# Performance work log

Measured on AMD Instinct MI355X. Metric: run time of the kernel, lower is better.

The kernel has to match this reference:

```python
import jax, jax.numpy as jnp
import numpy as np

B, N, T, FM = 2, 768, 96, 8
HID = 64
TD = HID // 2   # temporal_dim = max(8, 32) = 32
MD = HID // 2   # mark_hidden_dim = 32


def _lin_init(key, fan_in, fan_out):
    k1, k2 = jax.random.split(key)
    bound = 1.0 / np.sqrt(fan_in)
    w = jax.random.uniform(k1, (fan_in, fan_out), minval=-bound, maxval=bound, dtype=jnp.float32)
    b = jax.random.uniform(k2, (fan_out,), minval=-bound, maxval=bound, dtype=jnp.float32)
    return w, b


def setup_inputs() -> dict:
    key = jax.random.key(0)
    ks = jax.random.split(key, 16)
    x_hist = jax.random.normal(ks[0], (B, N, T), dtype=jnp.float32)
    x_mark = jax.random.normal(ks[1], (B, N, T, FM), dtype=jnp.float32)
    a_static = jax.random.uniform(ks[2], (N, N), dtype=jnp.float32)
    te_w1, te_b1 = _lin_init(ks[3], 3, TD)
    te_w2, te_b2 = _lin_init(ks[4], TD, TD)
    me_w1, me_b1 = _lin_init(ks[5], FM, MD)
    me_w2, me_b2 = _lin_init(ks[6], MD, MD)
    nf_w, nf_b = _lin_init(ks[7], TD + MD, HID)
    ps_w1, ps_b1 = _lin_init(ks[8], 3 * HID, HID)
    ps_w2, ps_b2 = _lin_init(ks[9], HID, 1)
    raw_lambda = jnp.array([np.log(0.1 / 0.9)], dtype=jnp.float32)  # logit(lambda_init)
    return dict(x_hist=x_hist, x_mark=x_mark, a_static=a_static,
                te_w1=te_w1, te_b1=te_b1, te_w2=te_w2, te_b2=te_b2,
                me_w1=me_w1, me_b1=me_b1, me_w2=me_w2, me_b2=me_b2,
                nf_w=nf_w, nf_b=nf_b,
                ps_w1=ps_w1, ps_b1=ps_b1, ps_w2=ps_w2, ps_b2=ps_b2,
                raw_lambda=raw_lambda)


def reference(x_hist, x_mark, a_static,
              te_w1, te_b1, te_w2, te_b2,
              me_w1, me_b1, me_w2, me_b2,
              nf_w, nf_b, ps_w1, ps_b1, ps_w2, ps_b2, raw_lambda):
    n = x_hist.shape[1]
    # temporal stats: last / mean / max over T -> [B,N,3]
    stats = jnp.stack([x_hist[:, :, -1], x_hist.mean(axis=-1), x_hist.max(axis=-1)], axis=-1)
    h_t = jax.nn.relu(stats @ te_w1 + te_b1) @ te_w2 + te_b2          # [B,N,TD]
    mark_sum = x_mark.mean(axis=2)                                    # [B,N,FM]
    h_m = jax.nn.relu(mark_sum @ me_w1 + me_b1) @ me_w2 + me_b2       # [B,N,MD]
    h = jax.nn.relu(jnp.concatenate([h_t, h_m], axis=-1) @ nf_w + nf_b)  # [B,N,H]
    # pair scorer: Linear([h_i, h_j, |h_i-h_j|]) decomposed over the 3 blocks
    hdim = h.shape[-1]
    w_i, w_j, w_d = ps_w1[:hdim], ps_w1[hdim:2 * hdim], ps_w1[2 * hdim:]
    s_i = h @ w_i                                                     # [B,N,H]
    s_j = h @ w_j                                                     # [B,N,H]
    diff = jnp.abs(h[:, :, None, :] - h[:, None, :, :])               # [B,N,N,H]
    pre = s_i[:, :, None, :] + s_j[:, None, :, :] + diff @ w_d + ps_b1
    delta = jnp.tanh((jax.nn.relu(pre) @ ps_w2 + ps_b2)[..., 0])      # [B,N,N]
    eye = jnp.eye(n, dtype=delta.dtype)
    delta = delta * (1.0 - eye)
    delta = 0.5 * (delta + jnp.swapaxes(delta, 1, 2))                 # sym_graph
    lam = jax.nn.sigmoid(raw_lambda)                                  # [1]
    a_hybrid = a_static[None] + lam * delta
    a_hybrid = jax.nn.relu(a_hybrid)                                  # nonneg_mode='relu'
    d = jnp.clip(a_hybrid.sum(axis=-1, keepdims=True), 1e-6, None)    # row norm
    a_hybrid = a_hybrid / d
    return a_hybrid, lam
```

## Files before the change

kernel.cpp:

```cpp
#include <hip/hip_runtime.h>
#include <hip/hip_bf16.h>
#include <math.h>

#define B_ 2
#define N_ 768
#define T_ 96
#define FM_ 8
#define HID_ 64
#define TD_ 32
#define MD_ 32
#define TILE 16
#define TI32 32
#define NTILES (N_/TILE)
#define PERB 600
#define SSTR 68

typedef __attribute__((ext_vector_type(8))) short short8v;
typedef __attribute__((ext_vector_type(4))) float f32x4;
typedef __attribute__((ext_vector_type(4))) unsigned int uint4v;

__device__ __forceinline__ unsigned int pack_bf2(float d0, float d1){
  __hip_bfloat162 t = __float22bfloat162_rn(make_float2(d0, d1));
  unsigned int u;
  __builtin_memcpy(&u, &t, 4);
  return u;
}

__device__ __forceinline__ float ftanh(float x){
  float e = __expf(2.f * x);
  return 1.f - 2.f * __builtin_amdgcn_rcpf(e + 1.f);
}

__device__ __forceinline__ float wave_sum64(float v){
  #pragma unroll
  for (int m = 32; m; m >>= 1) v += __shfl_xor(v, m);
  return v;
}
__device__ __forceinline__ float wave_max64(float v){
  #pragma unroll
  for (int m = 32; m; m >>= 1) v = fmaxf(v, __shfl_xor(v, m));
  return v;
}

__global__ __launch_bounds__(64) void feat_kernel(
    const float* __restrict__ x_hist, const float* __restrict__ x_mark,
    const float* __restrict__ te_w1, const float* __restrict__ te_b1,
    const float* __restrict__ te_w2, const float* __restrict__ te_b2,
    const float* __restrict__ me_w1, const float* __restrict__ me_b1,
    const float* __restrict__ me_w2, const float* __restrict__ me_b2,
    const float* __restrict__ nf_w,  const float* __restrict__ nf_b,
    const float* __restrict__ ps_w1,
    float* __restrict__ h_out, float* __restrict__ si_out, float* __restrict__ sj_out,
    unsigned short* __restrict__ wdf)
{
  const int lane = threadIdx.x;

  if (blockIdx.x >= B_ * N_) {
    const int q  = blockIdx.x - B_ * N_;
    const int nt = q >> 1, s = q & 1;
    const int col = (lane & 15) + 16 * nt;
    const int k0  = s * 32 + ((lane >> 4) << 3);
    #pragma unroll
    for (int jj = 0; jj < 8; ++jj) {
      float v = ps_w1[(2 * HID_ + k0 + jj) * HID_ + col];
      __hip_bfloat16 bv = __float2bfloat16(v);
      unsigned short us;
      __builtin_memcpy(&us, &bv, 2);
      wdf[(q * 64 + lane) * 8 + jj] = us;
    }
    return;
  }

  const int row = blockIdx.x;

  __shared__ float st[3];
  __shared__ float ms[FM_];
  __shared__ float t1s[TD_];
  __shared__ float m1s[MD_];
  __shared__ float hc[HID_];
  __shared__ float hs[HID_];

  const float* xh = x_hist + (long)row * T_;
  float s  = xh[lane];
  float mx = s;
  if (lane < T_ - 64) { float v = xh[lane + 64]; s += v; mx = fmaxf(mx, v); }
  s  = wave_sum64(s);
  mx = wave_max64(mx);
  if (lane == 0) { st[0] = xh[T_ - 1]; st[1] = s * (1.0f / T_); st[2] = mx; }

  const float* xm = x_mark + (long)row * T_ * FM_;
  float msv = 0.f;
  #pragma unroll
  for (int k = 0; k < 12; ++k) msv += xm[lane + 64 * k];
  msv += __shfl_xor(msv, 8);
  msv += __shfl_xor(msv, 16);
  msv += __shfl_xor(msv, 32);
  if (lane < FM_) ms[lane] = msv * (1.0f / T_);
  __syncthreads();

  if (lane < TD_) {
    float a = te_b1[lane];
    #pragma unroll
    for (int k = 0; k < 3; ++k) a += st[k] * te_w1[k * TD_ + lane];
    t1s[lane] = fmaxf(a, 0.f);
    float am = me_b1[lane];
    #pragma unroll
    for (int k = 0; k < FM_; ++k) am += ms[k] * me_w1[k * MD_ + lane];
    m1s[lane] = fmaxf(am, 0.f);
  }
  __syncthreads();
  if (lane < TD_) {
    float a = te_b2[lane];
    #pragma unroll
    for (int k = 0; k < TD_; ++k) a += t1s[k] * te_w2[k * TD_ + lane];
    hc[lane] = a;
    float am = me_b2[lane];
    #pragma unroll
    for (int k = 0; k < MD_; ++k) am += m1s[k] * me_w2[k * MD_ + lane];
    hc[TD_ + lane] = am;
  }
  __syncthreads();
  {
    float a = nf_b[lane];
    #pragma unroll
    for (int k = 0; k < HID_; ++k) a += hc[k] * nf_w[k * HID_ + lane];
    float hv = fmaxf(a, 0.f);
    hs[lane] = hv;
    h_out[(long)row * HID_ + lane] = hv;
  }
  __syncthreads();
  {
    float a1 = 0.f, a2 = 0.f;
    #pragma unroll
    for (int k = 0; k < HID_; ++k) {
      float hv = hs[k];
      a1 += hv * ps_w1[k * HID_ + lane];
      a2 += hv * ps_w1[(HID_ + k) * HID_ + lane];
    }
    si_out[(long)row * HID_ + lane] = a1;
    sj_out[(long)row * HID_ + lane] = a2;
  }
}

__global__ __launch_bounds__(256, 3) void pair_kernel(
    const float* __restrict__ h, const float* __restrict__ si, const float* __restrict__ sj,
    const float* __restrict__ ps_b1, const float* __restrict__ ps_w2,
    const float* __restrict__ ps_b2, const unsigned short* __restrict__ wdf,
    float* __restrict__ delta)
{
  int bidx = blockIdx.x;
  int b = bidx / PERB;
  int t = bidx % PERB;
  int a = 0;
  while (t >= NTILES - 2 * a) { t -= NTILES - 2 * a; ++a; }
  int tJ = 2 * a + t;
  const int i0 = a * TI32, j0 = tJ * TILE;

  __shared__ float hI  [TI32][HID_];
  __shared__ float hJT [HID_][TILE + 1];
  __shared__ float SIIb[TI32][SSTR];
  __shared__ float SJI_[TI32][SSTR];
  __shared__ float SIJb[TILE][SSTR];
  __shared__ float SJJ_[TILE][SSTR];
  __shared__ float w2s [HID_];

  const int tid  = threadIdx.x;
  const int lane = tid & 63;
  const int w    = tid >> 6;

  {
    const int r  = tid >> 4;
    const int c4 = (tid & 15) * 4;
    const f32x4 b14 = *(const f32x4*)(ps_b1 + c4);
    #pragma unroll
    for (int p = 0; p < 2; ++p) {
      const int rr = r + p * 16;
      const long gi = ((long)b * N_ + i0 + rr) * HID_ + c4;
      *(f32x4*)&hI  [rr][c4] = *(const f32x4*)(h  + gi);
      *(f32x4*)&SIIb[rr][c4] = *(const f32x4*)(si + gi) + b14;
      *(f32x4*)&SJI_[rr][c4] = *(const f32x4*)(sj + gi);
    }
    const long gj = ((long)b * N_ + j0 + r) * HID_ + c4;
    f32x4 vhj = *(const f32x4*)(h + gj);
    #pragma unroll
    for (int q = 0; q < 4; ++q) hJT[c4 + q][r] = vhj[q];
    *(f32x4*)&SIJb[r][c4] = *(const f32x4*)(si + gj) + b14;
    *(f32x4*)&SJJ_[r][c4] = *(const f32x4*)(sj + gj);
    if (tid < 16) *(f32x4*)&w2s[tid * 4] = *(const f32x4*)(ps_w2 + tid * 4);
  }
  const float b2 = ps_b2[0];
  __syncthreads();

  const int g   = lane >> 4;
  const int c16 = lane & 15;

  short8v wfr[8];
  const short8v* wdp = (const short8v*)wdf;
  #pragma unroll
  for (int q = 0; q < 8; ++q) wfr[q] = wdp[q * 64 + lane];

  float hJv[2][8];
  #pragma unroll
  for (int s = 0; s < 2; ++s)
    #pragma unroll
    for (int jj = 0; jj < 8; ++jj)
      hJv[s][jj] = hJT[32 * s + 8 * g + jj][c16];

  f32x4 sJJ4h[4], sIJ4h[4], w24h[4];
  #pragma unroll
  for (int mt = 0; mt < 4; ++mt) {
    const int cb = 16 * mt + 4 * g;
    sJJ4h[mt] = *(const f32x4*)&SJJ_[c16][cb];
    sIJ4h[mt] = *(const f32x4*)&SIJb[c16][cb];
    w24h[mt]  = *(const f32x4*)&w2s[cb];
  }

  float* drow = delta + (long)b * N_ * N_;

  #pragma unroll
  for (int m = 0; m < 8; ++m) {
    const int iloc = w * 8 + m;
    const int i = i0 + iloc;

    short8v afr[2];
    #pragma unroll
    for (int s = 0; s < 2; ++s) {
      f32x4 ha = *(const f32x4*)&hI[iloc][32 * s + 8 * g];
      f32x4 hb = *(const f32x4*)&hI[iloc][32 * s + 8 * g + 4];
      uint4v uv;
      #pragma unroll
      for (int p = 0; p < 2; ++p) {
        float d0 = fabsf(ha[2*p]   - hJv[s][2*p]);
        float d1 = fabsf(ha[2*p+1] - hJv[s][2*p+1]);
        uv[p] = pack_bf2(d0, d1);
      }
      #pragma unroll
      for (int p = 0; p < 2; ++p) {
        float d0 = fabsf(hb[2*p]   - hJv[s][4 + 2*p]);
        float d1 = fabsf(hb[2*p+1] - hJv[s][4 + 2*p+1]);
        uv[2 + p] = pack_bf2(d0, d1);
      }
      afr[s] = __builtin_bit_cast(short8v, uv);
    }

    f32x4 acc[4];
    #pragma unroll
    for (int mt = 0; mt < 4; ++mt) acc[mt] = (f32x4){0.f, 0.f, 0.f, 0.f};
    #pragma unroll
    for (int s = 0; s < 2; ++s)
      #pragma unroll
      for (int mt = 0; mt < 4; ++mt)
        acc[mt] = __builtin_amdgcn_mfma_f32_16x16x32_bf16(wfr[2 * mt + s], afr[s], acc[mt], 0, 0, 0);

    float a1 = 0.f, a2 = 0.f;
    #pragma unroll
    for (int mt = 0; mt < 4; ++mt) {
      const int cb = 16 * mt + 4 * g;
      f32x4 sII4 = *(const f32x4*)&SIIb[iloc][cb];
      f32x4 sJI4 = *(const f32x4*)&SJI_[iloc][cb];
      #pragma unroll
      for (int r = 0; r < 4; ++r) {
        float av = acc[mt][r];
        a1 += fmaxf(av + sII4[r] + sJJ4h[mt][r], 0.f) * w24h[mt][r];
        a2 += fmaxf(av + sJI4[r] + sIJ4h[mt][r], 0.f) * w24h[mt][r];
      }
    }
    a1 += __shfl_xor(a1, 16);  a1 += __shfl_xor(a1, 32);
    a2 += __shfl_xor(a2, 16);  a2 += __shfl_xor(a2, 32);

    if (g == 0) {
      const int j = j0 + c16;
      if (i < j) {
        float sym = 0.5f * (ftanh(a1 + b2) + ftanh(a2 + b2));
        drow[(long)i * N_ + j] = sym;
        drow[(long)j * N_ + i] = sym;
      } else if (i == j) {
        drow[(long)i * N_ + i] = 0.f;
      }
    }
  }
}

__global__ __launch_bounds__(256) void norm_kernel(
    const float* __restrict__ a_static, const float* __restrict__ raw_lambda,
    float* __restrict__ out)
{
  const int row = blockIdx.x;
  const int i   = row % N_;
  const int tid = threadIdx.x;
  const float lam = 1.f / (1.f + expf(-raw_lambda[0]));

  const float* arow = a_static + (long)i * N_;
  float* drow = out + (long)row * N_;

  float vals[3];
  float s = 0.f;
  #pragma unroll
  for (int r = 0; r < 3; ++r) {
    int j = r * 256 + tid;
    float v = arow[j] + lam * drow[j];
    v = fmaxf(v, 0.f);
    vals[r] = v;
    s += v;
  }
  s = wave_sum64(s);
  __shared__ float ps[4];
  if ((tid & 63) == 0) ps[tid >> 6] = s;
  __syncthreads();
  float tot = ps[0] + ps[1] + ps[2] + ps[3];
  float inv = 1.f / fmaxf(tot, 1e-6f);
  #pragma unroll
  for (int r = 0; r < 3; ++r) {
    int j = r * 256 + tid;
    drow[j] = vals[r] * inv;
  }
  if (row == 0 && tid == 0) out[(long)B_ * N_ * N_] = lam;
}

extern "C" void kernel_launch(void* const* d_in, const int* in_sizes, int n_in,
                              void* d_out, int out_size, void* d_ws, size_t ws_size,
                              hipStream_t stream) {
  const float* x_hist     = (const float*)d_in[0];
  const float* x_mark     = (const float*)d_in[1];
  const float* a_static   = (const float*)d_in[2];
  const float* te_w1      = (const float*)d_in[3];
  const float* te_b1      = (const float*)d_in[4];
  const float* te_w2      = (const float*)d_in[5];
  const float* te_b2      = (const float*)d_in[6];
  const float* me_w1      = (const float*)d_in[7];
  const float* me_b1      = (const float*)d_in[8];
  const float* me_w2      = (const float*)d_in[9];
  const float* me_b2      = (const float*)d_in[10];
  const float* nf_w       = (const float*)d_in[11];
  const float* nf_b       = (const float*)d_in[12];
  const float* ps_w1      = (const float*)d_in[13];
  const float* ps_b1      = (const float*)d_in[14];
  const float* ps_w2      = (const float*)d_in[15];
  const float* ps_b2      = (const float*)d_in[16];
  const float* raw_lambda = (const float*)d_in[17];

  float* out = (float*)d_out;
  float* h   = (float*)d_ws;
  float* si  = h  + (long)B_ * N_ * HID_;
  float* sj  = si + (long)B_ * N_ * HID_;
  unsigned short* wdf = (unsigned short*)(sj + (long)B_ * N_ * HID_);

  feat_kernel<<<B_ * N_ + 8, 64, 0, stream>>>(
      x_hist, x_mark, te_w1, te_b1, te_w2, te_b2,
      me_w1, me_b1, me_w2, me_b2, nf_w, nf_b, ps_w1, h, si, sj, wdf);

  pair_kernel<<<B_ * PERB, 256, 0, stream>>>(
      h, si, sj, ps_b1, ps_w2, ps_b2, wdf, out);

  norm_kernel<<<B_ * N_, 256, 0, stream>>>(a_static, raw_lambda, out);
}
```

Measured before the change: 35.60 us.

## Batch rows per block in feat and norm kernels, widen pair tiles

The feature kernel now runs 256-thread blocks, with each wave handling two rows and one block converting the bf16 weight fragments. The pair kernel processes two 16-column J halves per block, reusing the loaded I-tile and halving the block count. The norm kernel assigns one row per wave with float4 loads and stores, which removes the shared-memory reduction and block barrier. Together these cut launch and block overhead and redundant I-tile loads, in exchange for extra barriers inside the pair loop and less parallelism per block.

```diff
diff --git a/kernel.cpp b/kernel.cpp
--- a/kernel.cpp
+++ b/kernel.cpp
@@ -12,7 +12,7 @@
 #define TILE 16
 #define TI32 32
 #define NTILES (N_/TILE)
-#define PERB 600
+#define PERB2 300
 #define SSTR 68
 
 typedef __attribute__((ext_vector_type(8))) short short8v;
@@ -42,7 +42,7 @@
   return v;
 }
 
-__global__ __launch_bounds__(64) void feat_kernel(
+__global__ __launch_bounds__(256) void feat_kernel(
     const float* __restrict__ x_hist, const float* __restrict__ x_mark,
     const float* __restrict__ te_w1, const float* __restrict__ te_b1,
     const float* __restrict__ te_w2, const float* __restrict__ te_b2,
@@ -53,92 +53,101 @@
     float* __restrict__ h_out, float* __restrict__ si_out, float* __restrict__ sj_out,
     unsigned short* __restrict__ wdf)
 {
-  const int lane = threadIdx.x;
-
-  if (blockIdx.x >= B_ * N_) {
-    const int q  = blockIdx.x - B_ * N_;
-    const int nt = q >> 1, s = q & 1;
-    const int col = (lane & 15) + 16 * nt;
-    const int k0  = s * 32 + ((lane >> 4) << 3);
-    #pragma unroll
-    for (int jj = 0; jj < 8; ++jj) {
-      float v = ps_w1[(2 * HID_ + k0 + jj) * HID_ + col];
-      __hip_bfloat16 bv = __float2bfloat16(v);
-      unsigned short us;
-      __builtin_memcpy(&us, &bv, 2);
-      wdf[(q * 64 + lane) * 8 + jj] = us;
+  const int tid  = threadIdx.x;
+  const int lane = tid & 63;
+  const int w    = tid >> 6;
+  const int NBF  = (B_ * N_) / 8;
+
+  if (blockIdx.x >= NBF) {
+    #pragma unroll
+    for (int r2 = 0; r2 < 2; ++r2) {
+      const int q  = w * 2 + r2;
+      const int nt = q >> 1, s = q & 1;
+      const int col = (lane & 15) + 16 * nt;
+      const int k0  = s * 32 + ((lane >> 4) << 3);
+      #pragma unroll
+      for (int jj = 0; jj < 8; ++jj) {
+        float v = ps_w1[(2 * HID_ + k0 + jj) * HID_ + col];
+        __hip_bfloat16 bv = __float2bfloat16(v);
+        unsigned short us;
+        __builtin_memcpy(&us, &bv, 2);
+        wdf[(q * 64 + lane) * 8 + jj] = us;
+      }
     }
     return;
   }
 
-  const int row = blockIdx.x;
-
-  __shared__ float st[3];
-  __shared__ float ms[FM_];
-  __shared__ float t1s[TD_];
-  __shared__ float m1s[MD_];
-  __shared__ float hc[HID_];
-  __shared__ float hs[HID_];
-
-  const float* xh = x_hist + (long)row * T_;
-  float s  = xh[lane];
-  float mx = s;
-  if (lane < T_ - 64) { float v = xh[lane + 64]; s += v; mx = fmaxf(mx, v); }
-  s  = wave_sum64(s);
-  mx = wave_max64(mx);
-  if (lane == 0) { st[0] = xh[T_ - 1]; st[1] = s * (1.0f / T_); st[2] = mx; }
-
-  const float* xm = x_mark + (long)row * T_ * FM_;
-  float msv = 0.f;
-  #pragma unroll
-  for (int k = 0; k < 12; ++k) msv += xm[lane + 64 * k];
-  msv += __shfl_xor(msv, 8);
-  msv += __shfl_xor(msv, 16);
-  msv += __shfl_xor(msv, 32);
-  if (lane < FM_) ms[lane] = msv * (1.0f / T_);
-  __syncthreads();
-
-  if (lane < TD_) {
-    float a = te_b1[lane];
-    #pragma unroll
-    for (int k = 0; k < 3; ++k) a += st[k] * te_w1[k * TD_ + lane];
-    t1s[lane] = fmaxf(a, 0.f);
-    float am = me_b1[lane];
-    #pragma unroll
-    for (int k = 0; k < FM_; ++k) am += ms[k] * me_w1[k * MD_ + lane];
-    m1s[lane] = fmaxf(am, 0.f);
-  }
-  __syncthreads();
-  if (lane < TD_) {
-    float a = te_b2[lane];
-    #pragma unroll
-    for (int k = 0; k < TD_; ++k) a += t1s[k] * te_w2[k * TD_ + lane];
-    hc[lane] = a;
-    float am = me_b2[lane];
-    #pragma unroll
-    for (int k = 0; k < MD_; ++k) am += m1s[k] * me_w2[k * MD_ + lane];
-    hc[TD_ + lane] = am;
-  }
-  __syncthreads();
-  {
-    float a = nf_b[lane];
-    #pragma unroll
-    for (int k = 0; k < HID_; ++k) a += hc[k] * nf_w[k * HID_ + lane];
-    float hv = fmaxf(a, 0.f);
-    hs[lane] = hv;
-    h_out[(long)row * HID_ + lane] = hv;
-  }
-  __syncthreads();
-  {
-    float a1 = 0.f, a2 = 0.f;
-    #pragma unroll
-    for (int k = 0; k < HID_; ++k) {
-      float hv = hs[k];
-      a1 += hv * ps_w1[k * HID_ + lane];
-      a2 += hv * ps_w1[(HID_ + k) * HID_ + lane];
-    }
-    si_out[(long)row * HID_ + lane] = a1;
-    sj_out[(long)row * HID_ + lane] = a2;
+  __shared__ float st [4][3];
+  __shared__ float ms [4][FM_];
+  __shared__ float t1s[4][TD_];
+  __shared__ float m1s[4][MD_];
+  __shared__ float hc [4][HID_];
+  __shared__ float hs [4][HID_];
+
+  for (int r2 = 0; r2 < 2; ++r2) {
+    const int row = blockIdx.x * 8 + w * 2 + r2;
+
+    const float* xh = x_hist + (long)row * T_;
+    float s  = xh[lane];
+    float mx = s;
+    if (lane < T_ - 64) { float v = xh[lane + 64]; s += v; mx = fmaxf(mx, v); }
+    s  = wave_sum64(s);
+    mx = wave_max64(mx);
+    if (lane == 0) { st[w][0] = xh[T_ - 1]; st[w][1] = s * (1.0f / T_); st[w][2] = mx; }
+
+    const float* xm = x_mark + (long)row * T_ * FM_;
+    float msv = 0.f;
+    #pragma unroll
+    for (int k = 0; k < 12; ++k) msv += xm[lane + 64 * k];
+    msv += __shfl_xor(msv, 8);
+    msv += __shfl_xor(msv, 16);
+    msv += __shfl_xor(msv, 32);
+    if (lane < FM_) ms[w][lane] = msv * (1.0f / T_);
+    __syncthreads();
+
+    if (lane < TD_) {
+      float a = te_b1[lane];
+      #pragma unroll
+      for (int k = 0; k < 3; ++k) a += st[w][k] * te_w1[k * TD_ + lane];
+      t1s[w][lane] = fmaxf(a, 0.f);
+      float am = me_b1[lane];
+      #pragma unroll
+      for (int k = 0; k < FM_; ++k) am += ms[w][k] * me_w1[k * MD_ + lane];
+      m1s[w][lane] = fmaxf(am, 0.f);
+    }
+    __syncthreads();
+    if (lane < TD_) {
+      float a = te_b2[lane];
+      #pragma unroll
+      for (int k = 0; k < TD_; ++k) a += t1s[w][k] * te_w2[k * TD_ + lane];
+      hc[w][lane] = a;
+      float am = me_b2[lane];
+      #pragma unroll
+      for (int k = 0; k < MD_; ++k) am += m1s[w][k] * me_w2[k * MD_ + lane];
+      hc[w][TD_ + lane] = am;
+    }
+    __syncthreads();
+    {
+      float a = nf_b[lane];
+      #pragma unroll
+      for (int k = 0; k < HID_; ++k) a += hc[w][k] * nf_w[k * HID_ + lane];
+      float hv = fmaxf(a, 0.f);
+      hs[w][lane] = hv;
+      h_out[(long)row * HID_ + lane] = hv;
+    }
+    __syncthreads();
+    {
+      float a1 = 0.f, a2 = 0.f;
+      #pragma unroll
+      for (int k = 0; k < HID_; ++k) {
+        float hv = hs[w][k];
+        a1 += hv * ps_w1[k * HID_ + lane];
+        a2 += hv * ps_w1[(HID_ + k) * HID_ + lane];
+      }
+      si_out[(long)row * HID_ + lane] = a1;
+      sj_out[(long)row * HID_ + lane] = a2;
+    }
+    __syncthreads();
   }
 }
 
@@ -149,47 +158,38 @@
     float* __restrict__ delta)
 {
   int bidx = blockIdx.x;
-  int b = bidx / PERB;
-  int t = bidx % PERB;
+  int b = bidx / PERB2;
+  int t = bidx % PERB2;
   int a = 0;
-  while (t >= NTILES - 2 * a) { t -= NTILES - 2 * a; ++a; }
-  int tJ = 2 * a + t;
-  const int i0 = a * TI32, j0 = tJ * TILE;
+  while (t >= 24 - a) { t -= 24 - a; ++a; }
+  const int i0    = a * TI32;
+  const int jbase = TI32 * a + 32 * t;
 
   __shared__ float hI  [TI32][HID_];
-  __shared__ float hJT [HID_][TILE + 1];
   __shared__ float SIIb[TI32][SSTR];
   __shared__ float SJI_[TI32][SSTR];
+  __shared__ float w2s [HID_];
+  __shared__ float hJT [HID_][TILE + 1];
   __shared__ float SIJb[TILE][SSTR];
   __shared__ float SJJ_[TILE][SSTR];
-  __shared__ float w2s [HID_];
 
   const int tid  = threadIdx.x;
   const int lane = tid & 63;
   const int w    = tid >> 6;
-
-  {
-    const int r  = tid >> 4;
-    const int c4 = (tid & 15) * 4;
-    const f32x4 b14 = *(const f32x4*)(ps_b1 + c4);
-    #pragma unroll
-    for (int p = 0; p < 2; ++p) {
-      const int rr = r + p * 16;
-      const long gi = ((long)b * N_ + i0 + rr) * HID_ + c4;
-      *(f32x4*)&hI  [rr][c4] = *(const f32x4*)(h  + gi);
-      *(f32x4*)&SIIb[rr][c4] = *(const f32x4*)(si + gi) + b14;
-      *(f32x4*)&SJI_[rr][c4] = *(const f32x4*)(sj + gi);
-    }
-    const long gj = ((long)b * N_ + j0 + r) * HID_ + c4;
-    f32x4 vhj = *(const f32x4*)(h + gj);
-    #pragma unroll
-    for (int q = 0; q < 4; ++q) hJT[c4 + q][r] = vhj[q];
-    *(f32x4*)&SIJb[r][c4] = *(const f32x4*)(si + gj) + b14;
-    *(f32x4*)&SJJ_[r][c4] = *(const f32x4*)(sj + gj);
-    if (tid < 16) *(f32x4*)&w2s[tid * 4] = *(const f32x4*)(ps_w2 + tid * 4);
-  }
+  const int r    = tid >> 4;
+  const int c4   = (tid & 15) * 4;
+  const f32x4 b14 = *(const f32x4*)(ps_b1 + c4);
+
+  #pragma unroll
+  for (int p = 0; p < 2; ++p) {
+    const int rr = r + p * 16;
+    const long gi = ((long)b * N_ + i0 + rr) * HID_ + c4;
+    *(f32x4*)&hI  [rr][c4] = *(const f32x4*)(h  + gi);
+    *(f32x4*)&SIIb[rr][c4] = *(const f32x4*)(si + gi) + b14;
+    *(f32x4*)&SJI_[rr][c4] = *(const f32x4*)(sj + gi);
+  }
+  if (tid < 16) *(f32x4*)&w2s[tid * 4] = *(const f32x4*)(ps_w2 + tid * 4);
   const float b2 = ps_b2[0];
-  __syncthreads();
 
   const int g   = lane >> 4;
   const int c16 = lane & 15;
@@ -199,83 +199,98 @@
   #pragma unroll
   for (int q = 0; q < 8; ++q) wfr[q] = wdp[q * 64 + lane];
 
-  float hJv[2][8];
-  #pragma unroll
-  for (int s = 0; s < 2; ++s)
-    #pragma unroll
-    for (int jj = 0; jj < 8; ++jj)
-      hJv[s][jj] = hJT[32 * s + 8 * g + jj][c16];
-
-  f32x4 sJJ4h[4], sIJ4h[4], w24h[4];
-  #pragma unroll
-  for (int mt = 0; mt < 4; ++mt) {
-    const int cb = 16 * mt + 4 * g;
-    sJJ4h[mt] = *(const f32x4*)&SJJ_[c16][cb];
-    sIJ4h[mt] = *(const f32x4*)&SIJb[c16][cb];
-    w24h[mt]  = *(const f32x4*)&w2s[cb];
-  }
-
   float* drow = delta + (long)b * N_ * N_;
 
-  #pragma unroll
-  for (int m = 0; m < 8; ++m) {
-    const int iloc = w * 8 + m;
-    const int i = i0 + iloc;
-
-    short8v afr[2];
-    #pragma unroll
-    for (int s = 0; s < 2; ++s) {
-      f32x4 ha = *(const f32x4*)&hI[iloc][32 * s + 8 * g];
-      f32x4 hb = *(const f32x4*)&hI[iloc][32 * s + 8 * g + 4];
-      uint4v uv;
-      #pragma unroll
-      for (int p = 0; p < 2; ++p) {
-        float d0 = fabsf(ha[2*p]   - hJv[s][2*p]);
-        float d1 = fabsf(ha[2*p+1] - hJv[s][2*p+1]);
-        uv[p] = pack_bf2(d0, d1);
-      }
-      #pragma unroll
-      for (int p = 0; p < 2; ++p) {
-        float d0 = fabsf(hb[2*p]   - hJv[s][4 + 2*p]);
-        float d1 = fabsf(hb[2*p+1] - hJv[s][4 + 2*p+1]);
-        uv[2 + p] = pack_bf2(d0, d1);
-      }
-      afr[s] = __builtin_bit_cast(short8v, uv);
-    }
-
-    f32x4 acc[4];
-    #pragma unroll
-    for (int mt = 0; mt < 4; ++mt) acc[mt] = (f32x4){0.f, 0.f, 0.f, 0.f};
+  for (int half = 0; half < 2; ++half) {
+    const int j0 = jbase + 16 * half;
+
+    {
+      const long gj = ((long)b * N_ + j0 + r) * HID_ + c4;
+      f32x4 vhj = *(const f32x4*)(h + gj);
+      #pragma unroll
+      for (int q = 0; q < 4; ++q) hJT[c4 + q][r] = vhj[q];
+      *(f32x4*)&SIJb[r][c4] = *(const f32x4*)(si + gj) + b14;
+      *(f32x4*)&SJJ_[r][c4] = *(const f32x4*)(sj + gj);
+    }
+    __syncthreads();
+
+    float hJv[2][8];
     #pragma unroll
     for (int s = 0; s < 2; ++s)
       #pragma unroll
-      for (int mt = 0; mt < 4; ++mt)
-        acc[mt] = __builtin_amdgcn_mfma_f32_16x16x32_bf16(wfr[2 * mt + s], afr[s], acc[mt], 0, 0, 0);
-
-    float a1 = 0.f, a2 = 0.f;
+      for (int jj = 0; jj < 8; ++jj)
+        hJv[s][jj] = hJT[32 * s + 8 * g + jj][c16];
+
+    f32x4 sJJ4h[4], sIJ4h[4], w24h[4];
     #pragma unroll
     for (int mt = 0; mt < 4; ++mt) {
       const int cb = 16 * mt + 4 * g;
-      f32x4 sII4 = *(const f32x4*)&SIIb[iloc][cb];
-      f32x4 sJI4 = *(const f32x4*)&SJI_[iloc][cb];
-      #pragma unroll
-      for (int r = 0; r < 4; ++r) {
-        float av = acc[mt][r];
-        a1 += fmaxf(av + sII4[r] + sJJ4h[mt][r], 0.f) * w24h[mt][r];
-        a2 += fmaxf(av + sJI4[r] + sIJ4h[mt][r], 0.f) * w24h[mt][r];
-      }
-    }
-    a1 += __shfl_xor(a1, 16);  a1 += __shfl_xor(a1, 32);
-    a2 += __shfl_xor(a2, 16);  a2 += __shfl_xor(a2, 32);
-
-    if (g == 0) {
-      const int j = j0 + c16;
-      if (i < j) {
-        float sym = 0.5f * (ftanh(a1 + b2) + ftanh(a2 + b2));
-        drow[(long)i * N_ + j] = sym;
-        drow[(long)j * N_ + i] = sym;
-      } else if (i == j) {
-        drow[(long)i * N_ + i] = 0.f;
+      sJJ4h[mt] = *(const f32x4*)&SJJ_[c16][cb];
+      sIJ4h[mt] = *(const f32x4*)&SIJb[c16][cb];
+      w24h[mt]  = *(const f32x4*)&w2s[cb];
+    }
+    __syncthreads();
+
+    #pragma unroll
+    for (int m = 0; m < 8; ++m) {
+      const int iloc = w * 8 + m;
+      const int i = i0 + iloc;
+
+      short8v afr[2];
+      #pragma unroll
+      for (int s = 0; s < 2; ++s) {
+        f32x4 ha = *(const f32x4*)&hI[iloc][32 * s + 8 * g];
+        f32x4 hb = *(const f32x4*)&hI[iloc][32 * s + 8 * g + 4];
+        uint4v uv;
+        #pragma unroll
+        for (int p = 0; p < 2; ++p) {
+          float d0 = fabsf(ha[2*p]   - hJv[s][2*p]);
+          float d1 = fabsf(ha[2*p+1] - hJv[s][2*p+1]);
+          uv[p] = pack_bf2(d0, d1);
+        }
+        #pragma unroll
+        for (int p = 0; p < 2; ++p) {
+          float d0 = fabsf(hb[2*p]   - hJv[s][4 + 2*p]);
+          float d1 = fabsf(hb[2*p+1] - hJv[s][4 + 2*p+1]);
+          uv[2 + p] = pack_bf2(d0, d1);
+        }
+        afr[s] = __builtin_bit_cast(short8v, uv);
+      }
+
+      f32x4 acc[4];
+      #pragma unroll
+      for (int mt = 0; mt < 4; ++mt) acc[mt] = (f32x4){0.f, 0.f, 0.f, 0.f};
+      #pragma unroll
+      for (int s = 0; s < 2; ++s)
+        #pragma unroll
+        for (int mt = 0; mt < 4; ++mt)
+          acc[mt] = __builtin_amdgcn_mfma_f32_16x16x32_bf16(wfr[2 * mt + s], afr[s], acc[mt], 0, 0, 0);
+
+      float a1 = 0.f, a2 = 0.f;
+      #pragma unroll
+      for (int mt = 0; mt < 4; ++mt) {
+        const int cb = 16 * mt + 4 * g;
+        f32x4 sII4 = *(const f32x4*)&SIIb[iloc][cb];
+        f32x4 sJI4 = *(const f32x4*)&SJI_[iloc][cb];
+        #pragma unroll
+        for (int rr = 0; rr < 4; ++rr) {
+          float av = acc[mt][rr];
+          a1 += fmaxf(av + sII4[rr] + sJJ4h[mt][rr], 0.f) * w24h[mt][rr];
+          a2 += fmaxf(av + sJI4[rr] + sIJ4h[mt][rr], 0.f) * w24h[mt][rr];
+        }
+      }
+      a1 += __shfl_xor(a1, 16);  a1 += __shfl_xor(a1, 32);
+      a2 += __shfl_xor(a2, 16);  a2 += __shfl_xor(a2, 32);
+
+      if (g == 0) {
+        const int j = j0 + c16;
+        if (i < j) {
+          float sym = 0.5f * (ftanh(a1 + b2) + ftanh(a2 + b2));
+          drow[(long)i * N_ + j] = sym;
+          drow[(long)j * N_ + i] = sym;
+        } else if (i == j) {
+          drow[(long)i * N_ + i] = 0.f;
+        }
       }
     }
   }
@@ -285,36 +300,36 @@
     const float* __restrict__ a_static, const float* __restrict__ raw_lambda,
     float* __restrict__ out)
 {
-  const int row = blockIdx.x;
-  const int i   = row % N_;
-  const int tid = threadIdx.x;
+  const int tid  = threadIdx.x;
+  const int lane = tid & 63;
+  const int w    = tid >> 6;
+  const int row  = blockIdx.x * 4 + w;
+  const int i    = row % N_;
   const float lam = 1.f / (1.f + expf(-raw_lambda[0]));
 
   const float* arow = a_static + (long)i * N_;
   float* drow = out + (long)row * N_;
 
-  float vals[3];
+  f32x4 vals[3];
   float s = 0.f;
   #pragma unroll
   for (int r = 0; r < 3; ++r) {
-    int j = r * 256 + tid;
-    float v = arow[j] + lam * drow[j];
-    v = fmaxf(v, 0.f);
+    const int off = r * 256 + lane * 4;
+    f32x4 va = *(const f32x4*)(arow + off);
+    f32x4 vd = *(const f32x4*)(drow + off);
+    f32x4 v  = va + lam * vd;
+    v = __builtin_elementwise_max(v, (f32x4){0.f, 0.f, 0.f, 0.f});
     vals[r] = v;
-    s += v;
+    s += v[0] + v[1] + v[2] + v[3];
   }
   s = wave_sum64(s);
-  __shared__ float ps[4];
-  if ((tid & 63) == 0) ps[tid >> 6] = s;
-  __syncthreads();
-  float tot = ps[0] + ps[1] + ps[2] + ps[3];
-  float inv = 1.f / fmaxf(tot, 1e-6f);
+  float inv = 1.f / fmaxf(s, 1e-6f);
   #pragma unroll
   for (int r = 0; r < 3; ++r) {
-    int j = r * 256 + tid;
-    drow[j] = vals[r] * inv;
-  }
-  if (row == 0 && tid == 0) out[(long)B_ * N_ * N_] = lam;
+    const int off = r * 256 + lane * 4;
+    *(f32x4*)(drow + off) = vals[r] * inv;
+  }
+  if (row == 0 && lane == 0) out[(long)B_ * N_ * N_] = lam;
 }
 
 extern "C" void kernel_launch(void* const* d_in, const int* in_sizes, int n_in,
@@ -345,12 +360,12 @@
   float* sj  = si + (long)B_ * N_ * HID_;
   unsigned short* wdf = (unsigned short*)(sj + (long)B_ * N_ * HID_);
 
-  feat_kernel<<<B_ * N_ + 8, 64, 0, stream>>>(
+  feat_kernel<<<(B_ * N_) / 8 + 1, 256, 0, stream>>>(
       x_hist, x_mark, te_w1, te_b1, te_w2, te_b2,
       me_w1, me_b1, me_w2, me_b2, nf_w, nf_b, ps_w1, h, si, sj, wdf);
 
-  pair_kernel<<<B_ * PERB, 256, 0, stream>>>(
+  pair_kernel<<<B_ * PERB2, 256, 0, stream>>>(
       h, si, sj, ps_b1, ps_w2, ps_b2, wdf, out);
 
-  norm_kernel<<<B_ * N_, 256, 0, stream>>>(a_static, raw_lambda, out);
-}
+  norm_kernel<<<(B_ * N_) / 4, 256, 0, stream>>>(a_static, raw_lambda, out);
+}
```

New measurement: 66.20 us. 86.0% more time.
